# Kernel tuning notes

Hardware: AMD Instinct MI355X
Metric: run time of the kernel (lower is better)

Reference implementation:

```python
import jax, jax.numpy as jnp
import numpy as np
import math

BANDWIDTH = 0.1
_INV_SQRT_2PI = 1.0 / math.sqrt(2.0 * math.pi)


def setup_inputs() -> dict:
    key = jax.random.key(0)
    k1, k2 = jax.random.split(key)
    data = jax.random.normal(k1, (16, 32768), dtype=jnp.float32)
    c_X = jax.random.normal(k2, (256,), dtype=jnp.float32)
    return {"data": data, "dim": -1, "c_X": c_X}


def reference(data, dim, c_X):
    # data: [B, LEN] after moving `dim` to last axis; c_X: [K] grid points
    LEN = data.shape[dim]
    x = jnp.swapaxes(data, dim, -1)  # torch .transpose(dim, -1)
    inv_b = 1.0 / BANDWIDTH
    # res: [B, LEN, K] broadcasted pairwise differences
    z = (x[..., None] - c_X) * inv_b
    # standard normal pdf of z, scaled by 1/bandwidth
    pdf = (inv_b * _INV_SQRT_2PI) * jnp.exp(-0.5 * z * z)
    pdf = pdf.sum(axis=1) / LEN  # [B, K], mean over samples
    return pdf.T  # [K, B] per original permute(1, 0)
```

## Files before the change

kernel.cpp:

```cpp
#include <hip/hip_runtime.h>


constexpr int   BINS  = 3072;
constexpr float H     = 0.004f;
constexpr float INVH  = 250.0f;
constexpr float LO    = -6.144f;
constexpr float SFAC  = 8.49321736f;
constexpr int   QH    = 8;
constexpr int   NT    = 1024;
constexpr unsigned int POISON = 0xAAAAAAAAu;

__global__ __launch_bounds__(NT) void kde_fused(
    const float* __restrict__ data, const float* __restrict__ c_X,
    float* __restrict__ out, float* __restrict__ ws_part, int LEN, int B) {
  __shared__ unsigned int h[BINS];
  __shared__ float red[4][256];

  const int t = threadIdx.x;
  const int b = blockIdx.x & 15;
  const int q = blockIdx.x >> 4;

  const int seg = LEN / QH;
  const float4* src4 = (const float4*)(data + (size_t)b * LEN + (size_t)q * seg);
  const float4 x = src4[t];
  const int k = t & 255, part = t >> 8;
  const float c = c_X[k];

  if (t < BINS / 4) ((uint4*)h)[t] = uint4{0u, 0u, 0u, 0u};
  __syncthreads();

  {
    float v[4] = {x.x, x.y, x.z, x.w};
#pragma unroll
    for (int e = 0; e < 4; ++e) {
      float p = fmaf(v[e], INVH, -LO * INVH);
      p = fminf(fmaxf(p, 1.0f), (float)(BINS - 2));
      int          ib = (int)p;
      float        f  = p - (float)ib;
      unsigned int w1 = (unsigned int)(f * 32768.0f + 0.5f);
      atomicAdd(&h[ib], 32768u - w1);
      atomicAdd(&h[ib + 1], w1);
    }
  }
  __syncthreads();

  int m = (int)fmaf(c, INVH, -LO * INVH + 0.5f);
  int lo4 = ((m & ~3) - 128) >> 2;
  lo4 = max(0, min(BINS / 4 - 64, lo4));

  const float dt = H * SFAC;
  float tl = (fmaf((float)(lo4 * 4 + part * 64), H, LO) - c) * SFAC;

  const uint4* h4 = (const uint4*)h;
  const int base = lo4 + part * 16;
  float acc = 0.f;
#pragma unroll 4
  for (int j4 = 0; j4 < 16; ++j4) {
    uint4 w = h4[base + j4];
    float t0 = tl, t1 = tl + dt, t2 = tl + 2.f * dt, t3 = tl + 3.f * dt;
    acc = fmaf((float)w.x, __builtin_amdgcn_exp2f(-(t0 * t0)), acc);
    acc = fmaf((float)w.y, __builtin_amdgcn_exp2f(-(t1 * t1)), acc);
    acc = fmaf((float)w.z, __builtin_amdgcn_exp2f(-(t2 * t2)), acc);
    acc = fmaf((float)w.w, __builtin_amdgcn_exp2f(-(t3 * t3)), acc);
    tl += 4.f * dt;
  }
  red[part][k] = acc;
  __syncthreads();

  if (t >= 256) return;
  const float mine = (red[0][t] + red[1][t]) + (red[2][t] + red[3][t]);

  if (q != 0) {
    __hip_atomic_store(&ws_part[((size_t)b * QH + q) * 256 + t], mine,
                       __ATOMIC_RELAXED, __HIP_MEMORY_SCOPE_AGENT);
    return;
  }

  const unsigned int* p[QH - 1];
#pragma unroll
  for (int i = 0; i < QH - 1; ++i)
    p[i] = (const unsigned int*)&ws_part[((size_t)b * QH + (i + 1)) * 256 + t];

  unsigned int u[QH - 1];
  bool any;
  do {
#pragma unroll
    for (int i = 0; i < QH - 1; ++i)
      u[i] = __hip_atomic_load(p[i], __ATOMIC_RELAXED, __HIP_MEMORY_SCOPE_AGENT);
    any = false;
#pragma unroll
    for (int i = 0; i < QH - 1; ++i) any |= (u[i] == POISON);
    if (any) __builtin_amdgcn_s_sleep(1);
  } while (any);

  float s = mine;
#pragma unroll
  for (int i = 0; i < QH - 1; ++i) s += __uint_as_float(u[i]);

  const float norm = 3.98942280f / ((float)LEN * 32768.0f);
  out[(size_t)t * B + b] = s * norm;
}

extern "C" void kernel_launch(void* const* d_in, const int* in_sizes, int n_in,
                              void* d_out, int out_size, void* d_ws, size_t ws_size,
                              hipStream_t stream) {
  const float* data = (const float*)d_in[0];
  const float* c_X  = (const float*)d_in[2];
  float* out        = (float*)d_out;

  const int B   = 16;
  const int LEN = in_sizes[0] / B;

  float* ws_part = (float*)d_ws;

  kde_fused<<<dim3(16 * QH), NT, 0, stream>>>(data, c_X, out, ws_part, LEN, B);
}
```

Measured before the change: 61.00 us.

## Use nearest-bin histogram, narrower window, and wave-shuffle reduction

Replaces linear-interpolated binning (two LDS atomics per sample) with nearest-bin counting (one atomic per sample). The Gaussian evaluation window shrinks from 256 to 192 bins, and threads are remapped so the four partial sums for each grid point sit in adjacent lanes. Those partials are combined with shuffles, which removes the shared reduction array and one barrier. The aim is fewer LDS atomics and fewer exp evaluations, at the cost of more binning error and a truncated kernel tail (about 5.6 sigma, down from 7.5) that may affect accuracy.

Measured after the change: 59.95 us. No clear change (-1.7%).

```diff
diff --git a/kernel.cpp b/kernel.cpp
--- a/kernel.cpp
+++ b/kernel.cpp
@@ -8,13 +8,13 @@
 constexpr float SFAC  = 8.49321736f;
 constexpr int   QH    = 8;
 constexpr int   NT    = 1024;
+constexpr int   W4    = 12;
 constexpr unsigned int POISON = 0xAAAAAAAAu;
 
 __global__ __launch_bounds__(NT) void kde_fused(
     const float* __restrict__ data, const float* __restrict__ c_X,
     float* __restrict__ out, float* __restrict__ ws_part, int LEN, int B) {
   __shared__ unsigned int h[BINS];
-  __shared__ float red[4][256];
 
   const int t = threadIdx.x;
   const int b = blockIdx.x & 15;
@@ -23,7 +23,7 @@
   const int seg = LEN / QH;
   const float4* src4 = (const float4*)(data + (size_t)b * LEN + (size_t)q * seg);
   const float4 x = src4[t];
-  const int k = t & 255, part = t >> 8;
+  const int k = t >> 2, part = t & 3;
   const float c = c_X[k];
 
   if (t < BINS / 4) ((uint4*)h)[t] = uint4{0u, 0u, 0u, 0u};
@@ -33,29 +33,25 @@
     float v[4] = {x.x, x.y, x.z, x.w};
 #pragma unroll
     for (int e = 0; e < 4; ++e) {
-      float p = fmaf(v[e], INVH, -LO * INVH);
-      p = fminf(fmaxf(p, 1.0f), (float)(BINS - 2));
-      int          ib = (int)p;
-      float        f  = p - (float)ib;
-      unsigned int w1 = (unsigned int)(f * 32768.0f + 0.5f);
-      atomicAdd(&h[ib], 32768u - w1);
-      atomicAdd(&h[ib + 1], w1);
+      float p = fmaf(v[e], INVH, -LO * INVH + 0.5f);
+      p = fminf(fmaxf(p, 0.0f), (float)(BINS - 1));
+      atomicAdd(&h[(int)p], 1u);
     }
   }
   __syncthreads();
 
   int m = (int)fmaf(c, INVH, -LO * INVH + 0.5f);
-  int lo4 = ((m & ~3) - 128) >> 2;
-  lo4 = max(0, min(BINS / 4 - 64, lo4));
+  int lo4 = (m >> 2) - 24;
+  lo4 = max(0, min(BINS / 4 - 4 * W4, lo4));
 
   const float dt = H * SFAC;
-  float tl = (fmaf((float)(lo4 * 4 + part * 64), H, LO) - c) * SFAC;
+  float tl = (fmaf((float)(lo4 * 4 + part * (4 * W4)), H, LO) - c) * SFAC;
 
   const uint4* h4 = (const uint4*)h;
-  const int base = lo4 + part * 16;
+  const int base = lo4 + part * W4;
   float acc = 0.f;
-#pragma unroll 4
-  for (int j4 = 0; j4 < 16; ++j4) {
+#pragma unroll
+  for (int j4 = 0; j4 < W4; ++j4) {
     uint4 w = h4[base + j4];
     float t0 = tl, t1 = tl + dt, t2 = tl + 2.f * dt, t3 = tl + 3.f * dt;
     acc = fmaf((float)w.x, __builtin_amdgcn_exp2f(-(t0 * t0)), acc);
@@ -64,14 +60,13 @@
     acc = fmaf((float)w.w, __builtin_amdgcn_exp2f(-(t3 * t3)), acc);
     tl += 4.f * dt;
   }
-  red[part][k] = acc;
-  __syncthreads();
 
-  if (t >= 256) return;
-  const float mine = (red[0][t] + red[1][t]) + (red[2][t] + red[3][t]);
+  acc += __shfl_xor(acc, 1, 64);
+  acc += __shfl_xor(acc, 2, 64);
+  if (part != 0) return;
 
   if (q != 0) {
-    __hip_atomic_store(&ws_part[((size_t)b * QH + q) * 256 + t], mine,
+    __hip_atomic_store(&ws_part[((size_t)b * QH + q) * 256 + k], acc,
                        __ATOMIC_RELAXED, __HIP_MEMORY_SCOPE_AGENT);
     return;
   }
@@ -79,7 +74,7 @@
   const unsigned int* p[QH - 1];
 #pragma unroll
   for (int i = 0; i < QH - 1; ++i)
-    p[i] = (const unsigned int*)&ws_part[((size_t)b * QH + (i + 1)) * 256 + t];
+    p[i] = (const unsigned int*)&ws_part[((size_t)b * QH + (i + 1)) * 256 + k];
 
   unsigned int u[QH - 1];
   bool any;
@@ -93,12 +88,12 @@
     if (any) __builtin_amdgcn_s_sleep(1);
   } while (any);
 
-  float s = mine;
+  float s = acc;
 #pragma unroll
   for (int i = 0; i < QH - 1; ++i) s += __uint_as_float(u[i]);
 
-  const float norm = 3.98942280f / ((float)LEN * 32768.0f);
-  out[(size_t)t * B + b] = s * norm;
+  const float norm = 3.98942280f / (float)LEN;
+  out[(size_t)k * B + b] = s * norm;
 }
 
 extern "C" void kernel_launch(void* const* d_in, const int* in_sizes, int n_in,
```
